# Optimization experiments

Measured on AMD Instinct MI355X. Metric: run time of the kernel, lower is better.

Reference implementation:

```python
import jax, jax.numpy as jnp
import numpy as np

E = 128      # embed_dim
NH = 4       # num_heads
HD = E // NH # head_dim = 32
ND = 5       # num_domains
LN_EPS = 1e-5


def setup_inputs() -> dict:
    key = jax.random.key(0)
    ks = jax.random.split(key, 16)
    B, C, D, H, W = 4, 128, 32, 64, 64
    s = 0.02
    return {
        "x": jax.random.normal(ks[0], (B, C, D, H, W), dtype=jnp.float32),
        "domain_idx": jax.random.randint(ks[1], (B,), 0, ND),
        "emb": jax.random.normal(ks[2], (ND, E), dtype=jnp.float32) * s,
        "q_proj_w": jax.random.normal(ks[3], (E, E), dtype=jnp.float32) * s,
        "q_proj_b": jnp.zeros((E,), jnp.float32),
        "wq": jax.random.normal(ks[4], (E, E), dtype=jnp.float32) * s,
        "bq": jnp.zeros((E,), jnp.float32),
        "wk": jax.random.normal(ks[5], (E, E), dtype=jnp.float32) * s,
        "bk": jnp.zeros((E,), jnp.float32),
        "wv": jax.random.normal(ks[6], (E, E), dtype=jnp.float32) * s,
        "bv": jnp.zeros((E,), jnp.float32),
        "wo": jax.random.normal(ks[7], (E, E), dtype=jnp.float32) * s,
        "bo": jnp.zeros((E,), jnp.float32),
        "ln_g": jnp.ones((E,), jnp.float32),
        "ln_b": jnp.zeros((E,), jnp.float32),
    }


def reference(x, domain_idx, emb, q_proj_w, q_proj_b, wq, bq, wk, bk, wv, bv,
              wo, bo, ln_g, ln_b):
    B, C, D, H, W = x.shape
    xr = x.reshape(B, C, -1).transpose(0, 2, 1)          # (B, N, C) tokens
    # single query from domain embedding
    de = emb[domain_idx]                                  # (B, E)
    q = de @ q_proj_w.T + q_proj_b                        # nn.Linear
    # MHA projections (torch nn.MultiheadAttention semantics)
    qh = (q @ wq.T + bq).reshape(B, NH, HD)               # (B, NH, HD)
    kh = (xr @ wk.T + bk).reshape(B, -1, NH, HD)          # (B, N, NH, HD)
    vh = (xr @ wv.T + bv).reshape(B, -1, NH, HD)
    scale = 1.0 / jnp.sqrt(jnp.float32(HD))
    scores = jnp.einsum('bhd,bnhd->bhn', qh, kh) * scale  # (B, NH, N)
    attn = jax.nn.softmax(scores, axis=-1)
    ctx = jnp.einsum('bhn,bnhd->bhd', attn, vh).reshape(B, E)
    out = ctx @ wo.T + bo                                 # (B, E) single token
    # LayerNorm of the single attended vector (broadcast over N is identical)
    mu = jnp.mean(out, axis=-1, keepdims=True)
    var = jnp.mean((out - mu) ** 2, axis=-1, keepdims=True)
    ln = (out - mu) * jax.lax.rsqrt(var + LN_EPS) * ln_g + ln_b
    xr = xr + ln[:, None, :]                              # residual broadcast-add
    return xr.transpose(0, 2, 1).reshape(B, C, D, H, W)
```

## Files before the change

kernel.cpp:

```cpp
#include <hip/hip_runtime.h>
#include <math.h>

#define E 128
#define NH 4
#define HD 32
#define LN_EPS 1e-5f
#define CHN 64
#define BPB 128
#define PW 129

#define BAR_LGKM()    do { asm volatile("s_waitcnt lgkmcnt(0)" ::: "memory"); __builtin_amdgcn_s_barrier(); } while (0)
#define BAR_VM_LGKM() do { asm volatile("s_waitcnt vmcnt(0) lgkmcnt(0)" ::: "memory"); __builtin_amdgcn_s_barrier(); } while (0)

typedef const __attribute__((address_space(1))) void* gas_p;
typedef __attribute__((address_space(3))) void* las_p;
__device__ __forceinline__ void gload_lds16(const float* g, void* l) {
    __builtin_amdgcn_global_load_lds((gas_p)(const void*)g, (las_p)l, 16, 0, 0);
}

typedef float f32x4 __attribute__((ext_vector_type(4)));

__global__ __launch_bounds__(512)
void k0_prep(const int* __restrict__ didx,
             const float* __restrict__ emb,
             const float* __restrict__ qpw, const float* __restrict__ qpb,
             const float* __restrict__ wq, const float* __restrict__ bq,
             const float* __restrict__ wk,
             float* __restrict__ u_s, int B)
{
    __shared__ float wbuf[E * PW];
    __shared__ float de_sh[4][E];
    __shared__ float q_sh[4][E];
    __shared__ float qh_sh[4][E];
    __shared__ int didx_sh[8];
    const int t = threadIdx.x;
    const int bb = t >> 7, c = t & 127;
    const float scale = 0.17677669529663687f;
    if (t < B) didx_sh[t] = didx[t];
    __syncthreads();
    for (int b0 = 0; b0 < B; b0 += 4) {
        const int b = b0 + bb;
        const bool act = b < B;
        if (act) de_sh[bb][c] = emb[(long)didx_sh[b] * E + c];
        for (int i = t; i < E * E; i += 512) wbuf[(i >> 7) * PW + (i & 127)] = qpw[i];
        __syncthreads();
        if (act) {
            float a = qpb[c];
            for (int j = 0; j < E; ++j) a += wbuf[c * PW + j] * de_sh[bb][j];
            q_sh[bb][c] = a;
        }
        __syncthreads();
        for (int i = t; i < E * E; i += 512) wbuf[(i >> 7) * PW + (i & 127)] = wq[i];
        __syncthreads();
        if (act) {
            float a = bq[c];
            for (int j = 0; j < E; ++j) a += wbuf[c * PW + j] * q_sh[bb][j];
            qh_sh[bb][c] = a;
        }
        __syncthreads();
        for (int i = t; i < E * E; i += 512) wbuf[(i >> 7) * PW + (i & 127)] = wk[i];
        __syncthreads();
        if (act) {
            #pragma unroll
            for (int h = 0; h < NH; ++h) {
                float a = 0.f;
                for (int d = 0; d < HD; ++d)
                    a += qh_sh[bb][h * HD + d] * wbuf[(h * HD + d) * PW + c];
                u_s[((long)b * NH + h) * E + c] = a * scale;
            }
        }
        __syncthreads();
    }
}

__global__ __launch_bounds__(256, 2)
void kA_attn(const float* __restrict__ x, const float* __restrict__ u_s,
             float* __restrict__ part_ctx, float* __restrict__ part_l,
             int N, int nk)
{
    __shared__ float4 tile[2][2048];
    __shared__ __align__(16) float p_sh[NH][CHN];
    __shared__ __align__(16) float red_sh[4][16][20];
    __shared__ float lacc[4][NH];

    const int t = threadIdx.x;
    const int lane = t & 63;
    const int wvid = t >> 6;
    const int g = blockIdx.x;
    const int b = g >> 7;
    const int bi = g & 127;

    const int q    = t & 15;
    const int cseg = t >> 4;
    const int th   = t & 15;
    const int n2   = ((t >> 4) << 2) | (th >> 2);
    const int h2   = th & 3;

    auto STAGE = [&](int kk, int buf) {
        const float* xb = x + (long)b * E * N + (long)(bi * nk + kk) * CHN;
        float4* tb = &tile[buf][0];
        #pragma unroll
        for (int r = 0; r < 8; ++r) {
            const int sbase = ((r << 2) + wvid) << 6;
            const int s = sbase + lane;
            const int c = s >> 4, qg = s & 15;
            gload_lds16(xb + (long)c * N + (qg << 2), (void*)&tb[sbase]);
        }
    };

    float u_reg[8][NH];
    #pragma unroll
    for (int j = 0; j < 8; ++j)
        #pragma unroll
        for (int hh = 0; hh < NH; ++hh)
            u_reg[j][hh] = u_s[((long)b * NH + hh) * E + (cseg << 3) + j];

    float l_loc = 0.f;
    float acc[NH][8];
    #pragma unroll
    for (int hh = 0; hh < NH; ++hh)
        #pragma unroll
        for (int j = 0; j < 8; ++j) acc[hh][j] = 0.f;

    STAGE(0, 0);
    BAR_VM_LGKM();
    int cur = 0;

    for (int k = 0; k < nk; ++k) {
        if (k + 1 < nk) STAGE(k + 1, cur ^ 1);
        const float4* lt = &tile[cur][0];

        float4 xc[8];
        float sa[4][NH];
        #pragma unroll
        for (int tok = 0; tok < 4; ++tok)
            #pragma unroll
            for (int hh = 0; hh < NH; ++hh) sa[tok][hh] = 0.f;
        #pragma unroll
        for (int j = 0; j < 8; ++j) {
            float4 xq = lt[(((cseg << 3) + j) << 4) + q];
            xc[j] = xq;
            #pragma unroll
            for (int hh = 0; hh < NH; ++hh) {
                const float uv = u_reg[j][hh];
                sa[0][hh] = fmaf(uv, xq.x, sa[0][hh]);
                sa[1][hh] = fmaf(uv, xq.y, sa[1][hh]);
                sa[2][hh] = fmaf(uv, xq.z, sa[2][hh]);
                sa[3][hh] = fmaf(uv, xq.w, sa[3][hh]);
            }
        }
        #pragma unroll
        for (int tok = 0; tok < 4; ++tok)
            #pragma unroll
            for (int hh = 0; hh < NH; ++hh) {
                sa[tok][hh] += __shfl_xor(sa[tok][hh], 16);
                sa[tok][hh] += __shfl_xor(sa[tok][hh], 32);
            }
        if (lane < 16) {
            *(float4*)&red_sh[wvid][q][0]  = make_float4(sa[0][0], sa[0][1], sa[0][2], sa[0][3]);
            *(float4*)&red_sh[wvid][q][4]  = make_float4(sa[1][0], sa[1][1], sa[1][2], sa[1][3]);
            *(float4*)&red_sh[wvid][q][8]  = make_float4(sa[2][0], sa[2][1], sa[2][2], sa[2][3]);
            *(float4*)&red_sh[wvid][q][12] = make_float4(sa[3][0], sa[3][1], sa[3][2], sa[3][3]);
        }
        BAR_LGKM();

        float s = red_sh[0][t >> 4][th] + red_sh[1][t >> 4][th]
                + red_sh[2][t >> 4][th] + red_sh[3][t >> 4][th];
        float p = __expf(s);
        l_loc += p;
        p_sh[h2][n2] = p;
        BAR_LGKM();

        float4 pq[NH];
        #pragma unroll
        for (int hh = 0; hh < NH; ++hh) pq[hh] = *(const float4*)&p_sh[hh][q << 2];
        #pragma unroll
        for (int j = 0; j < 8; ++j) {
            const float4 xq = xc[j];
            #pragma unroll
            for (int hh = 0; hh < NH; ++hh) {
                float a = acc[hh][j];
                a = fmaf(pq[hh].x, xq.x, a); a = fmaf(pq[hh].y, xq.y, a);
                a = fmaf(pq[hh].z, xq.z, a); a = fmaf(pq[hh].w, xq.w, a);
                acc[hh][j] = a;
            }
        }
        BAR_VM_LGKM();
        cur ^= 1;
    }

    #pragma unroll
    for (int hh = 0; hh < NH; ++hh) {
        #pragma unroll
        for (int j = 0; j < 8; ++j) {
            float v = acc[hh][j];
            v += __shfl_xor(v, 1); v += __shfl_xor(v, 2);
            v += __shfl_xor(v, 4); v += __shfl_xor(v, 8);
            if (q == 0)
                part_ctx[((long)g * NH + hh) * E + (cseg << 3) + j] = v;
        }
    }
    float r = l_loc;
    r += __shfl_xor(r, 4); r += __shfl_xor(r, 8);
    r += __shfl_xor(r, 16); r += __shfl_xor(r, 32);
    if (lane < 4) lacc[wvid][lane] = r;
    __syncthreads();
    if (t < NH) {
        float L = 0.f;
        #pragma unroll
        for (int w = 0; w < 4; ++w) L += lacc[w][t];
        part_l[g * NH + t] = L;
    }
}

__global__ __launch_bounds__(512)
void kC_combine_outln(const float* __restrict__ part_ctx,
                      const float* __restrict__ part_l,
                      const float* __restrict__ wvw, const float* __restrict__ bv,
                      const float* __restrict__ wo, const float* __restrict__ bo,
                      const float* __restrict__ lng, const float* __restrict__ lnb,
                      float* __restrict__ ln_out)
{
    const int b = blockIdx.x;
    const int t = threadIdx.x;
    const int lane = t & 63, wv = t >> 6;
    __shared__ float Lsh[8][NH];
    __shared__ float invl_sh[NH];
    __shared__ float sctx[NH][E];
    __shared__ float ctxv[E];
    __shared__ float wbuf[E * PW];
    __shared__ float partred[4][128];
    __shared__ float vec1_sh[128];
    __shared__ float red512[512];

    {
        float pl = part_l[(b * BPB + (t >> 2)) * NH + (t & 3)];
        float r = pl;
        r += __shfl_xor(r, 4); r += __shfl_xor(r, 8);
        r += __shfl_xor(r, 16); r += __shfl_xor(r, 32);
        if (lane < 4) Lsh[wv][lane] = r;
    }
    __syncthreads();
    if (t < NH) {
        float L = 0.f;
        #pragma unroll
        for (int w = 0; w < 8; ++w) L += Lsh[w][t];
        invl_sh[t] = 1.f / L;
    }
    __syncthreads();

    {
        const int hB = t >> 7, cB = t & 127;
        const float* pc = part_ctx + (long)b * BPB * NH * E;
        float a0 = 0.f, a1 = 0.f, a2 = 0.f, a3 = 0.f;
        for (int i = 0; i < BPB; i += 4) {
            a0 += pc[((i + 0) * NH + hB) * E + cB];
            a1 += pc[((i + 1) * NH + hB) * E + cB];
            a2 += pc[((i + 2) * NH + hB) * E + cB];
            a3 += pc[((i + 3) * NH + hB) * E + cB];
        }
        sctx[hB][cB] = (a0 + a1 + a2 + a3) * invl_sh[hB];
    }
    __syncthreads();

    for (int i = t; i < E * E; i += 512) wbuf[(i >> 7) * PW + (i & 127)] = wvw[i];
    __syncthreads();
    const int rr = t & 127, qt = t >> 7;
    {
        const int hR = rr >> 5;
        float pa = 0.f;
        #pragma unroll
        for (int c2 = 0; c2 < 32; ++c2)
            pa = fmaf(wbuf[rr * PW + qt * 32 + c2], sctx[hR][qt * 32 + c2], pa);
        partred[qt][rr] = pa;
    }
    __syncthreads();
    if (t < 128)
        vec1_sh[t] = bv[t] + partred[0][t] + partred[1][t] + partred[2][t] + partred[3][t];
    __syncthreads();
    for (int i = t; i < E * E; i += 512) wbuf[(i >> 7) * PW + (i & 127)] = wo[i];
    __syncthreads();
    {
        float po = 0.f;
        #pragma unroll
        for (int c2 = 0; c2 < 32; ++c2)
            po = fmaf(wbuf[rr * PW + qt * 32 + c2], vec1_sh[qt * 32 + c2], po);
        partred[qt][rr] = po;
    }
    __syncthreads();
    float ov = 0.f;
    if (t < 128) ov = bo[t] + partred[0][t] + partred[1][t] + partred[2][t] + partred[3][t];
    red512[t] = (t < 128) ? ov : 0.f;
    __syncthreads();
    for (int st = 64; st > 0; st >>= 1) { if (t < st) red512[t] += red512[t + st]; __syncthreads(); }
    const float mu = red512[0] * (1.f / E);
    __syncthreads();
    const float d = (t < 128) ? (ov - mu) : 0.f;
    red512[t] = d * d;
    __syncthreads();
    for (int st = 64; st > 0; st >>= 1) { if (t < st) red512[t] += red512[t + st]; __syncthreads(); }
    const float var = red512[0] * (1.f / E);
    if (t < 128) ln_out[b * E + t] = d * rsqrtf(var + LN_EPS) * lng[t] + lnb[t];
}

__global__ void k5_resid(const float* __restrict__ x, const float* __restrict__ ln,
                         float* __restrict__ out, int sh2, long total4)
{
    long i = (long)blockIdx.x * blockDim.x + threadIdx.x;
    const long stride = (long)gridDim.x * blockDim.x;
    for (; i < total4; i += stride) {
        const int bc = (int)(i >> sh2);
        const float l = ln[bc];
        f32x4 v = ((const f32x4*)x)[i];
        v += l;
        __builtin_nontemporal_store(v, ((f32x4*)out) + i);
    }
}

extern "C" void kernel_launch(void* const* d_in, const int* in_sizes, int n_in,
                              void* d_out, int out_size, void* d_ws, size_t ws_size,
                              hipStream_t stream) {
    const float* x   = (const float*)d_in[0];
    const int*   didx= (const int*)d_in[1];
    const float* emb = (const float*)d_in[2];
    const float* qpw = (const float*)d_in[3];
    const float* qpb = (const float*)d_in[4];
    const float* wq  = (const float*)d_in[5];
    const float* bq  = (const float*)d_in[6];
    const float* wk  = (const float*)d_in[7];
    const float* wvw = (const float*)d_in[9];
    const float* bv  = (const float*)d_in[10];
    const float* wo  = (const float*)d_in[11];
    const float* bo  = (const float*)d_in[12];
    const float* lng = (const float*)d_in[13];
    const float* lnb = (const float*)d_in[14];
    float* out = (float*)d_out;

    const int B = in_sizes[1];
    const long totalx = (long)in_sizes[0];
    const int N = (int)(totalx / ((long)B * E));
    const int nk = N / (CHN * BPB);
    int lgN = 0; while ((1 << lgN) < N) ++lgN;
    const int sh2 = lgN - 2;

    float* ws       = (float*)d_ws;
    float* u_s      = ws;
    float* part_l   = u_s      + (long)B * NH * E;
    float* part_ctx = part_l   + (long)B * BPB * NH;
    float* ln_o     = part_ctx + (long)B * BPB * NH * E;

    k0_prep<<<1, 512, 0, stream>>>(didx, emb, qpw, qpb, wq, bq, wk, u_s, B);

    kA_attn<<<B * BPB, 256, 0, stream>>>(x, u_s, part_ctx, part_l, N, nk);

    kC_combine_outln<<<B, 512, 0, stream>>>(part_ctx, part_l,
                                            wvw, bv, wo, bo, lng, lnb, ln_o);

    long total4 = (long)B * E * N / 4;
    k5_resid<<<2048, 256, 0, stream>>>(x, ln_o, out, sh2, total4);
}
```

Baseline: 162.3 us.

## Run attention, combine and residual per batch so x stays cache-resident

Replaces the single whole-tensor launch sequence with a loop over batches. Each batch gets its own attention, combine and residual-add launches, and BPB is raised so one batch's attention grid still fills the GPU. The goal is for the residual pass to re-read a 64MB slice of x from the last-level cache rather than HBM, since it runs right after that slice's attention pass. The cost is several times more kernel launches, a single-block combine that now reduces four times as many partials serially, and less overlap between batches.

```diff
diff --git a/kernel.cpp b/kernel.cpp
--- a/kernel.cpp
+++ b/kernel.cpp
@@ -6,7 +6,7 @@
 #define HD 32
 #define LN_EPS 1e-5f
 #define CHN 64
-#define BPB 128
+#define BPB 512
 #define PW 129
 
 #define BAR_LGKM()    do { asm volatile("s_waitcnt lgkmcnt(0)" ::: "memory"); __builtin_amdgcn_s_barrier(); } while (0)
@@ -76,7 +76,7 @@
 __global__ __launch_bounds__(256, 2)
 void kA_attn(const float* __restrict__ x, const float* __restrict__ u_s,
              float* __restrict__ part_ctx, float* __restrict__ part_l,
-             int N, int nk)
+             int N, int b, int nk)
 {
     __shared__ float4 tile[2][2048];
     __shared__ __align__(16) float p_sh[NH][CHN];
@@ -86,9 +86,7 @@
     const int t = threadIdx.x;
     const int lane = t & 63;
     const int wvid = t >> 6;
-    const int g = blockIdx.x;
-    const int b = g >> 7;
-    const int bi = g & 127;
+    const int bi = blockIdx.x;
 
     const int q    = t & 15;
     const int cseg = t >> 4;
@@ -189,6 +187,7 @@
         cur ^= 1;
     }
 
+    const long pbase = ((long)(b * BPB + bi)) * NH;
     #pragma unroll
     for (int hh = 0; hh < NH; ++hh) {
         #pragma unroll
@@ -197,7 +196,7 @@
             v += __shfl_xor(v, 1); v += __shfl_xor(v, 2);
             v += __shfl_xor(v, 4); v += __shfl_xor(v, 8);
             if (q == 0)
-                part_ctx[((long)g * NH + hh) * E + (cseg << 3) + j] = v;
+                part_ctx[(pbase + hh) * E + (cseg << 3) + j] = v;
         }
     }
     float r = l_loc;
@@ -209,7 +208,7 @@
         float L = 0.f;
         #pragma unroll
         for (int w = 0; w < 4; ++w) L += lacc[w][t];
-        part_l[g * NH + t] = L;
+        part_l[pbase + t] = L;
     }
 }
 
@@ -219,26 +218,27 @@
                       const float* __restrict__ wvw, const float* __restrict__ bv,
                       const float* __restrict__ wo, const float* __restrict__ bo,
                       const float* __restrict__ lng, const float* __restrict__ lnb,
-                      float* __restrict__ ln_out)
+                      float* __restrict__ ln_out, int b)
 {
-    const int b = blockIdx.x;
     const int t = threadIdx.x;
     const int lane = t & 63, wv = t >> 6;
     __shared__ float Lsh[8][NH];
     __shared__ float invl_sh[NH];
     __shared__ float sctx[NH][E];
-    __shared__ float ctxv[E];
     __shared__ float wbuf[E * PW];
     __shared__ float partred[4][128];
     __shared__ float vec1_sh[128];
     __shared__ float red512[512];
 
     {
-        float pl = part_l[(b * BPB + (t >> 2)) * NH + (t & 3)];
-        float r = pl;
-        r += __shfl_xor(r, 4); r += __shfl_xor(r, 8);
-        r += __shfl_xor(r, 16); r += __shfl_xor(r, 32);
-        if (lane < 4) Lsh[wv][lane] = r;
+        const f32x4* pl4 = (const f32x4*)(part_l + (long)b * BPB * NH);
+        f32x4 r = pl4[t];
+        #pragma unroll
+        for (int o = 1; o < 64; o <<= 1) {
+            r.x += __shfl_xor(r.x, o); r.y += __shfl_xor(r.y, o);
+            r.z += __shfl_xor(r.z, o); r.w += __shfl_xor(r.w, o);
+        }
+        if (lane == 0) { Lsh[wv][0] = r.x; Lsh[wv][1] = r.y; Lsh[wv][2] = r.z; Lsh[wv][3] = r.w; }
     }
     __syncthreads();
     if (t < NH) {
@@ -303,17 +303,20 @@
     if (t < 128) ln_out[b * E + t] = d * rsqrtf(var + LN_EPS) * lng[t] + lnb[t];
 }
 
-__global__ void k5_resid(const float* __restrict__ x, const float* __restrict__ ln,
-                         float* __restrict__ out, int sh2, long total4)
+__global__ __launch_bounds__(256)
+void kB_resid(const float* __restrict__ x, const float* __restrict__ ln,
+              float* __restrict__ out, int sh2, int b, long total4b)
 {
+    const long base4 = (long)b * total4b;
     long i = (long)blockIdx.x * blockDim.x + threadIdx.x;
     const long stride = (long)gridDim.x * blockDim.x;
-    for (; i < total4; i += stride) {
-        const int bc = (int)(i >> sh2);
-        const float l = ln[bc];
-        f32x4 v = ((const f32x4*)x)[i];
-        v += l;
-        __builtin_nontemporal_store(v, ((f32x4*)out) + i);
+    const int boff = b * E;
+    for (; i < total4b; i += stride) {
+        const int c = (int)(i >> sh2);
+        const float lnv = ln[boff + c];
+        f32x4 v = ((const f32x4*)x)[base4 + i];
+        v += lnv;
+        __builtin_nontemporal_store(v, ((f32x4*)out) + base4 + i);
     }
 }
 
@@ -351,11 +354,11 @@
 
     k0_prep<<<1, 512, 0, stream>>>(didx, emb, qpw, qpb, wq, bq, wk, u_s, B);
 
-    kA_attn<<<B * BPB, 256, 0, stream>>>(x, u_s, part_ctx, part_l, N, nk);
-
-    kC_combine_outln<<<B, 512, 0, stream>>>(part_ctx, part_l,
-                                            wvw, bv, wo, bo, lng, lnb, ln_o);
-
-    long total4 = (long)B * E * N / 4;
-    k5_resid<<<2048, 256, 0, stream>>>(x, ln_o, out, sh2, total4);
-}
+    const long total4b = (long)E * N / 4;
+    for (int b = 0; b < B; ++b) {
+        kA_attn<<<BPB, 256, 0, stream>>>(x, u_s, part_ctx, part_l, N, b, nk);
+        kC_combine_outln<<<1, 512, 0, stream>>>(part_ctx, part_l,
+                                                wvw, bv, wo, bo, lng, lnb, ln_o, b);
+        kB_resid<<<2048, 256, 0, stream>>>(x, ln_o, out, sh2, b, total4b);
+    }
+}
```

After: 266.1 us. +64.0%, slower.

## Halve attention chunk size and deepen LDS prefetch pipeline to four buffers

Applied to the files above, without the earlier changes.

The attention kernel now processes 32-token chunks instead of 64 and keeps three async global-to-LDS loads in flight using a 4-slot ring buffer. Partial vmcnt waits replace the full drain at the end of each iteration, which removes one barrier per iteration. Thread-to-data mapping changes to 8 lanes per channel row with an extra shuffle stage, and only 128 threads compute exp. The goal is more memory-latency hiding on a bandwidth-bound streaming pass, at the cost of more iterations and more barriers per token.

```diff
diff --git a/kernel.cpp b/kernel.cpp
--- a/kernel.cpp
+++ b/kernel.cpp
@@ -5,12 +5,12 @@
 #define NH 4
 #define HD 32
 #define LN_EPS 1e-5f
-#define CHN 64
+#define CHN 32
+#define NBUF 4
 #define BPB 128
 #define PW 129
 
 #define BAR_LGKM()    do { asm volatile("s_waitcnt lgkmcnt(0)" ::: "memory"); __builtin_amdgcn_s_barrier(); } while (0)
-#define BAR_VM_LGKM() do { asm volatile("s_waitcnt vmcnt(0) lgkmcnt(0)" ::: "memory"); __builtin_amdgcn_s_barrier(); } while (0)
 
 typedef const __attribute__((address_space(1))) void* gas_p;
 typedef __attribute__((address_space(3))) void* las_p;
@@ -78,9 +78,9 @@
              float* __restrict__ part_ctx, float* __restrict__ part_l,
              int N, int nk)
 {
-    __shared__ float4 tile[2][2048];
+    __shared__ float4 tile[NBUF][1024];
     __shared__ __align__(16) float p_sh[NH][CHN];
-    __shared__ __align__(16) float red_sh[4][16][20];
+    __shared__ __align__(16) float red_sh[4][8][20];
     __shared__ float lacc[4][NH];
 
     const int t = threadIdx.x;
@@ -90,55 +90,58 @@
     const int b = g >> 7;
     const int bi = g & 127;
 
-    const int q    = t & 15;
-    const int cseg = t >> 4;
-    const int th   = t & 15;
-    const int n2   = ((t >> 4) << 2) | (th >> 2);
-    const int h2   = th & 3;
+    const int q    = t & 7;
+    const int cseg = t >> 3;
 
     auto STAGE = [&](int kk, int buf) {
         const float* xb = x + (long)b * E * N + (long)(bi * nk + kk) * CHN;
         float4* tb = &tile[buf][0];
         #pragma unroll
-        for (int r = 0; r < 8; ++r) {
+        for (int r = 0; r < 4; ++r) {
             const int sbase = ((r << 2) + wvid) << 6;
             const int s = sbase + lane;
-            const int c = s >> 4, qg = s & 15;
+            const int c = s >> 3, qg = s & 7;
             gload_lds16(xb + (long)c * N + (qg << 2), (void*)&tb[sbase]);
         }
     };
 
-    float u_reg[8][NH];
+    float u_reg[4][NH];
     #pragma unroll
-    for (int j = 0; j < 8; ++j)
+    for (int j = 0; j < 4; ++j)
         #pragma unroll
         for (int hh = 0; hh < NH; ++hh)
-            u_reg[j][hh] = u_s[((long)b * NH + hh) * E + (cseg << 3) + j];
+            u_reg[j][hh] = u_s[((long)b * NH + hh) * E + (cseg << 2) + j];
 
     float l_loc = 0.f;
-    float acc[NH][8];
+    float acc[NH][4];
     #pragma unroll
     for (int hh = 0; hh < NH; ++hh)
         #pragma unroll
-        for (int j = 0; j < 8; ++j) acc[hh][j] = 0.f;
-
-    STAGE(0, 0);
-    BAR_VM_LGKM();
-    int cur = 0;
+        for (int j = 0; j < 4; ++j) acc[hh][j] = 0.f;
+
+    STAGE(0, 0); __builtin_amdgcn_sched_barrier(0);
+    STAGE(1, 1); __builtin_amdgcn_sched_barrier(0);
+    STAGE(2, 2); __builtin_amdgcn_sched_barrier(0);
 
     for (int k = 0; k < nk; ++k) {
-        if (k + 1 < nk) STAGE(k + 1, cur ^ 1);
-        const float4* lt = &tile[cur][0];
-
-        float4 xc[8];
+        if (k + 2 < nk)      asm volatile("s_waitcnt vmcnt(8) lgkmcnt(0)" ::: "memory");
+        else if (k + 1 < nk) asm volatile("s_waitcnt vmcnt(4) lgkmcnt(0)" ::: "memory");
+        else                 asm volatile("s_waitcnt vmcnt(0) lgkmcnt(0)" ::: "memory");
+        __builtin_amdgcn_s_barrier();
+        __builtin_amdgcn_sched_barrier(0);
+        if (k + 3 < nk) { STAGE(k + 3, (k + 3) & 3); __builtin_amdgcn_sched_barrier(0); }
+
+        const float4* lt = &tile[k & 3][0];
+
+        float4 xc[4];
         float sa[4][NH];
         #pragma unroll
         for (int tok = 0; tok < 4; ++tok)
             #pragma unroll
             for (int hh = 0; hh < NH; ++hh) sa[tok][hh] = 0.f;
         #pragma unroll
-        for (int j = 0; j < 8; ++j) {
-            float4 xq = lt[(((cseg << 3) + j) << 4) + q];
+        for (int j = 0; j < 4; ++j) {
+            float4 xq = lt[(((cseg << 2) + j) << 3) + q];
             xc[j] = xq;
             #pragma unroll
             for (int hh = 0; hh < NH; ++hh) {
@@ -153,29 +156,33 @@
         for (int tok = 0; tok < 4; ++tok)
             #pragma unroll
             for (int hh = 0; hh < NH; ++hh) {
+                sa[tok][hh] += __shfl_xor(sa[tok][hh], 8);
                 sa[tok][hh] += __shfl_xor(sa[tok][hh], 16);
                 sa[tok][hh] += __shfl_xor(sa[tok][hh], 32);
             }
-        if (lane < 16) {
-            *(float4*)&red_sh[wvid][q][0]  = make_float4(sa[0][0], sa[0][1], sa[0][2], sa[0][3]);
-            *(float4*)&red_sh[wvid][q][4]  = make_float4(sa[1][0], sa[1][1], sa[1][2], sa[1][3]);
-            *(float4*)&red_sh[wvid][q][8]  = make_float4(sa[2][0], sa[2][1], sa[2][2], sa[2][3]);
-            *(float4*)&red_sh[wvid][q][12] = make_float4(sa[3][0], sa[3][1], sa[3][2], sa[3][3]);
+        if (lane < 8) {
+            *(float4*)&red_sh[wvid][lane][0]  = make_float4(sa[0][0], sa[0][1], sa[0][2], sa[0][3]);
+            *(float4*)&red_sh[wvid][lane][4]  = make_float4(sa[1][0], sa[1][1], sa[1][2], sa[1][3]);
+            *(float4*)&red_sh[wvid][lane][8]  = make_float4(sa[2][0], sa[2][1], sa[2][2], sa[2][3]);
+            *(float4*)&red_sh[wvid][lane][12] = make_float4(sa[3][0], sa[3][1], sa[3][2], sa[3][3]);
         }
         BAR_LGKM();
 
-        float s = red_sh[0][t >> 4][th] + red_sh[1][t >> 4][th]
-                + red_sh[2][t >> 4][th] + red_sh[3][t >> 4][th];
-        float p = __expf(s);
-        l_loc += p;
-        p_sh[h2][n2] = p;
+        if (t < 128) {
+            const int tokq = t >> 4, th = t & 15;
+            float s = red_sh[0][tokq][th] + red_sh[1][tokq][th]
+                    + red_sh[2][tokq][th] + red_sh[3][tokq][th];
+            float p = __expf(s);
+            l_loc += p;
+            p_sh[th & 3][(tokq << 2) | (th >> 2)] = p;
+        }
         BAR_LGKM();
 
         float4 pq[NH];
         #pragma unroll
         for (int hh = 0; hh < NH; ++hh) pq[hh] = *(const float4*)&p_sh[hh][q << 2];
         #pragma unroll
-        for (int j = 0; j < 8; ++j) {
+        for (int j = 0; j < 4; ++j) {
             const float4 xq = xc[j];
             #pragma unroll
             for (int hh = 0; hh < NH; ++hh) {
@@ -185,19 +192,16 @@
                 acc[hh][j] = a;
             }
         }
-        BAR_VM_LGKM();
-        cur ^= 1;
     }
 
     #pragma unroll
     for (int hh = 0; hh < NH; ++hh) {
         #pragma unroll
-        for (int j = 0; j < 8; ++j) {
+        for (int j = 0; j < 4; ++j) {
             float v = acc[hh][j];
-            v += __shfl_xor(v, 1); v += __shfl_xor(v, 2);
-            v += __shfl_xor(v, 4); v += __shfl_xor(v, 8);
+            v += __shfl_xor(v, 1); v += __shfl_xor(v, 2); v += __shfl_xor(v, 4);
             if (q == 0)
-                part_ctx[((long)g * NH + hh) * E + (cseg << 3) + j] = v;
+                part_ctx[((long)g * NH + hh) * E + (cseg << 2) + j] = v;
         }
     }
     float r = l_loc;
@@ -227,7 +231,6 @@
     __shared__ float Lsh[8][NH];
     __shared__ float invl_sh[NH];
     __shared__ float sctx[NH][E];
-    __shared__ float ctxv[E];
     __shared__ float wbuf[E * PW];
     __shared__ float partred[4][128];
     __shared__ float vec1_sh[128];
```

Result: slower. 185.9 us (+14.6%).
